# Optimization experiments

Hardware: AMD Instinct MI355X
Metric: run time of the kernel (lower is better)

The kernel has to match this reference:

```python
import jax, jax.numpy as jnp
import numpy as np

B, N, DIM, H, K = 2, 8192, 256, 8, 32
HD = DIM // H


def setup_inputs() -> dict:
    key = jax.random.key(0)
    ks = jax.random.split(key, 10)
    s = 1.0 / np.sqrt(DIM)
    return {
        "x": jax.random.normal(ks[0], (B, N, DIM), jnp.float32),
        "xyz": jax.random.normal(ks[1], (B, N, 3), jnp.float32),
        "idx": jax.random.randint(ks[2], (B, N, K), 0, N, jnp.int32),
        "Wq": jax.random.normal(ks[3], (DIM, DIM), jnp.float32) * s,
        "bq": jnp.zeros((DIM,), jnp.float32),
        "Wk": jax.random.normal(ks[4], (DIM, DIM), jnp.float32) * s,
        "bk": jnp.zeros((DIM,), jnp.float32),
        "Wv": jax.random.normal(ks[5], (DIM, DIM), jnp.float32) * s,
        "bv": jnp.zeros((DIM,), jnp.float32),
        "Wo": jax.random.normal(ks[6], (DIM, DIM), jnp.float32) * s,
        "bo": jnp.zeros((DIM,), jnp.float32),
        "W1": jax.random.normal(ks[7], (3, 32), jnp.float32) * 0.5,
        "b1": jnp.zeros((32,), jnp.float32),
        "W2": jax.random.normal(ks[8], (32, H), jnp.float32) * 0.2,
        "b2": jnp.zeros((H,), jnp.float32),
    }


def reference(x, xyz, idx, Wq, bq, Wk, bk, Wv, bv, Wo, bo, W1, b1, W2, b2):
    Bn, Nn, C = x.shape
    k = idx.shape[-1]
    q = (x @ Wq + bq).reshape(Bn, Nn, H, HD)          # [B,N,H,hd]
    kf = (x @ Wk + bk).reshape(Bn, Nn, H, HD)
    vf = (x @ Wv + bv).reshape(Bn, Nn, H, HD)
    # gather k neighbors per point (per-batch fancy indexing)
    gather = jax.vmap(lambda f, i: f[i])               # [N,H,hd],[N,k] -> [N,k,H,hd]
    kn = gather(kf, idx)                               # [B,N,k,H,hd]
    vn = gather(vf, idx)
    nxyz = jax.vmap(lambda p, i: p[i])(xyz, idx)       # [B,N,k,3]
    rel = xyz[:, :, None, :] - nxyz                    # [B,N,k,3]
    bias = jax.nn.relu(rel @ W1 + b1) @ W2 + b2        # [B,N,k,H]
    scores = jnp.einsum('bnhd,bnkhd->bnhk', q, kn) / np.sqrt(HD).astype(np.float32)
    scores = scores + bias.transpose(0, 1, 3, 2)       # [B,N,H,k]
    attn = jax.nn.softmax(scores, axis=-1)
    out = jnp.einsum('bnhk,bnkhd->bnhd', attn, vn).reshape(Bn, Nn, C)
    return out @ Wo + bo
```

## Files before the change

kernel.cpp:

```cpp
#include <hip/hip_runtime.h>
#include <hip/hip_bf16.h>

typedef unsigned int uint32;
typedef unsigned short ushort;
typedef __attribute__((ext_vector_type(4))) float floatx4;
typedef __attribute__((ext_vector_type(8))) __bf16 bf16x8;

#define NPTS 8192

__device__ __forceinline__ ushort f2bf(float f) {
    uint32 u = __float_as_uint(f);
    uint32 r = (u + 0x7fffu + ((u >> 16) & 1u)) >> 16;
    return (ushort)r;
}
__device__ __forceinline__ float bf1(ushort u) { return __uint_as_float((uint32)u << 16); }
__device__ __forceinline__ float bflo(uint32 u) { return __uint_as_float(u << 16); }
__device__ __forceinline__ float bfhi(uint32 u) { return __uint_as_float(u & 0xffff0000u); }

__global__ __launch_bounds__(256) void prep_kernel(
    const float* __restrict__ x, const float* __restrict__ xyz, const int* __restrict__ idx,
    const float* __restrict__ Wq, const float* __restrict__ Wk,
    const float* __restrict__ Wv, const float* __restrict__ Wo,
    const float* __restrict__ bq, const float* __restrict__ bk, const float* __restrict__ bv,
    const float* __restrict__ W1, const float* __restrict__ b1,
    const float* __restrict__ W2, const float* __restrict__ b2,
    ushort* __restrict__ xb, ushort* __restrict__ Wqkvt, ushort* __restrict__ Wot,
    float* __restrict__ biasqkv, ushort* __restrict__ bias_g) {
    const int bi = blockIdx.x;
    const int tid = threadIdx.x;
    if (bi < 4096) {
        int i = (bi * 256 + tid) * 4;
        float4 v = *(const float4*)(x + i);
        ushort4 o;
        o.x = f2bf(v.x); o.y = f2bf(v.y); o.z = f2bf(v.z); o.w = f2bf(v.w);
        *(ushort4*)(xb + i) = o;
    } else if (bi < 5120) {
        int f = (bi - 4096) * 256 + tid;
        if (f < 768 * 256) {
            int n = f >> 8, k = f & 255;
            int seg = n >> 8, nc = n & 255;
            const float* W = (seg == 0) ? Wq : (seg == 1) ? Wk : Wv;
            Wqkvt[f] = f2bf(W[k * 256 + nc]);
        } else {
            int g = f - 768 * 256;
            int n = g >> 8, k = g & 255;
            Wot[g] = f2bf(Wo[k * 256 + n]);
        }
        if (f < 768) biasqkv[f] = (f < 256) ? bq[f] : (f < 512) ? bk[f - 256] : bv[f - 512];
    } else {
        __shared__ float W1s[96], b1s[32], W2s[256], b2s[8];
        if (tid < 96) W1s[tid] = W1[tid];
        if (tid < 32) b1s[tid] = b1[tid];
        W2s[tid] = W2[tid];
        if (tid < 8) b2s[tid] = b2[tid];
        __syncthreads();
        const int wid = tid >> 6, lane = tid & 63;
        const int s = lane >> 5, j = lane & 31;
        const int p = (bi - 5120) * 8 + wid * 2 + s;
        const int b = p >> 13, n = p & 8191;
        const int nj = idx[(size_t)p * 32 + j];
        const size_t pb = ((size_t)b * NPTS + n) * 3;
        const size_t nb = ((size_t)b * NPTS + nj) * 3;
        const float rx = xyz[pb + 0] - xyz[nb + 0];
        const float ry = xyz[pb + 1] - xyz[nb + 1];
        const float rz = xyz[pb + 2] - xyz[nb + 2];
        float acc[8];
#pragma unroll
        for (int h = 0; h < 8; ++h) acc[h] = b2s[h];
#pragma unroll
        for (int u = 0; u < 32; ++u) {
            float hv = rx * W1s[u] + ry * W1s[32 + u] + rz * W1s[64 + u] + b1s[u];
            hv = fmaxf(hv, 0.f);
#pragma unroll
            for (int h = 0; h < 8; ++h) acc[h] += hv * W2s[u * 8 + h];
        }
#pragma unroll
        for (int h = 0; h < 8; ++h) bias_g[((size_t)p * 8 + h) * 32 + j] = f2bf(acc[h]);
    }
}

__global__ __launch_bounds__(256) void gemm_qkv(const ushort* __restrict__ A,
                                                const ushort* __restrict__ Wt,
                                                const float* __restrict__ bias,
                                                ushort* __restrict__ outp) {
    __shared__ __align__(16) ushort As[128 * 64];
    __shared__ __align__(16) ushort Bs[128 * 64];
    const int tid = threadIdx.x;
    const int w = tid >> 6, lane = tid & 63;
    const int m0 = blockIdx.y * 128, n0 = blockIdx.x * 128;
    const int wm = (w & 1) * 64, wn = (w >> 1) * 64;
    const int N = 768;

    floatx4 acc[4][4] = {};

    for (int kt = 0; kt < 256; kt += 64) {
        __syncthreads();
#pragma unroll
        for (int c4 = 0; c4 < 4; ++c4) {
            const int c = w * 4 + c4;
            const int r = c * 8 + (lane >> 3);
            const int gseg = (lane & 7) ^ (r & 7);
            const char* ga = (const char*)(A + (size_t)(m0 + r) * 256 + kt) + gseg * 16;
            const char* gb = (const char*)(Wt + (size_t)(n0 + r) * 256 + kt) + gseg * 16;
            __builtin_amdgcn_global_load_lds((const __attribute__((address_space(1))) void*)ga,
                                             (__attribute__((address_space(3))) void*)((char*)As + c * 1024),
                                             16, 0, 0);
            __builtin_amdgcn_global_load_lds((const __attribute__((address_space(1))) void*)gb,
                                             (__attribute__((address_space(3))) void*)((char*)Bs + c * 1024),
                                             16, 0, 0);
        }
        __syncthreads();

        bf16x8 af[2][4], bg[2][4];
#pragma unroll
        for (int kk = 0; kk < 2; ++kk) {
            const int s = kk * 4 + (lane >> 4);
            const int phys = s ^ (lane & 7);
#pragma unroll
            for (int i = 0; i < 4; ++i) {
                af[kk][i] = *(const bf16x8*)((const char*)As + (wm + i * 16 + (lane & 15)) * 128 + phys * 16);
                bg[kk][i] = *(const bf16x8*)((const char*)Bs + (wn + i * 16 + (lane & 15)) * 128 + phys * 16);
            }
        }
#pragma unroll
        for (int kk = 0; kk < 2; ++kk)
#pragma unroll
            for (int mi = 0; mi < 4; ++mi)
#pragma unroll
                for (int ni = 0; ni < 4; ++ni)
                    acc[mi][ni] = __builtin_amdgcn_mfma_f32_16x16x32_bf16(af[kk][mi], bg[kk][ni], acc[mi][ni], 0, 0, 0);
    }

#pragma unroll
    for (int ni = 0; ni < 4; ++ni) {
        const int col = n0 + wn + ni * 16 + (lane & 15);
        const float bv = bias[col];
#pragma unroll
        for (int mi = 0; mi < 4; ++mi) {
            const int row0 = m0 + wm + mi * 16 + (lane >> 4) * 4;
#pragma unroll
            for (int r = 0; r < 4; ++r)
                outp[(size_t)(row0 + r) * N + col] = f2bf(acc[mi][ni][r] + bv);
        }
    }
}

__global__ __launch_bounds__(256) void gemm_mfma64(const ushort* __restrict__ A,
                                                   const ushort* __restrict__ Wt,
                                                   const float* __restrict__ bias,
                                                   float* __restrict__ outv, int N) {
    __shared__ __align__(16) ushort As[64 * 32];
    __shared__ __align__(16) ushort Bs[64 * 32];
    const int tid = threadIdx.x;
    const int w = tid >> 6, lane = tid & 63;
    const int m0 = blockIdx.y * 64, n0 = blockIdx.x * 64;
    const int row = tid >> 2;
    const int col16 = (tid & 3) * 16;

    floatx4 acc[4] = {};

    for (int kt = 0; kt < 256; kt += 32) {
        __syncthreads();
        {
            const char* ga = (const char*)(A + (size_t)(m0 + row) * 256 + kt) + col16;
            const char* gb = (const char*)(Wt + (size_t)(n0 + row) * 256 + kt) + col16;
            __builtin_amdgcn_global_load_lds((const __attribute__((address_space(1))) void*)ga,
                                             (__attribute__((address_space(3))) void*)((char*)As + w * 1024),
                                             16, 0, 0);
            __builtin_amdgcn_global_load_lds((const __attribute__((address_space(1))) void*)gb,
                                             (__attribute__((address_space(3))) void*)((char*)Bs + w * 1024),
                                             16, 0, 0);
        }
        __syncthreads();

        bf16x8 af = *(const bf16x8*)&As[(w * 16 + (lane & 15)) * 32 + (lane >> 4) * 8];
        bf16x8 bg[4];
#pragma unroll
        for (int ni = 0; ni < 4; ++ni)
            bg[ni] = *(const bf16x8*)&Bs[(ni * 16 + (lane & 15)) * 32 + (lane >> 4) * 8];
#pragma unroll
        for (int ni = 0; ni < 4; ++ni)
            acc[ni] = __builtin_amdgcn_mfma_f32_16x16x32_bf16(af, bg[ni], acc[ni], 0, 0, 0);
    }

#pragma unroll
    for (int ni = 0; ni < 4; ++ni) {
        const int col = n0 + ni * 16 + (lane & 15);
        const float bv = bias[col];
        const int row0 = m0 + w * 16 + (lane >> 4) * 4;
#pragma unroll
        for (int r = 0; r < 4; ++r)
            outv[(size_t)(row0 + r) * N + col] = acc[ni][r] + bv;
    }
}

__global__ __launch_bounds__(256) void attn_kernel(
    const ushort* __restrict__ qkv, const int* __restrict__ idx,
    const ushort* __restrict__ bias_g, ushort* __restrict__ out) {
    __shared__ __align__(16) float q_s[4][2][32];
    __shared__ float e_s[4][2][32];
    __shared__ uint32 off_s[4][2][32];
    __shared__ float ssum_s[4][2];

    const int tid = threadIdx.x, wid = tid >> 6, lane = tid & 63;
    const int h = blockIdx.x & 7;
    const int pg = blockIdx.x >> 3;
    const int pbase = pg * 8 + wid * 2;
    const char* base = (const char*)qkv;

    const int s = lane >> 5, j = lane & 31;
    const int p = pbase + s;
    const int b = p >> 13;

    off_s[wid][s][j] = (uint32)(idx[(size_t)p * 32 + j] + b * NPTS) * 1536u;
    q_s[wid][s][j] = bf1(qkv[(size_t)p * 768 + h * 32 + j]);
    __syncthreads();

    {
        const uint4* kp = (const uint4*)(base + off_s[wid][s][j] + 512 + h * 64);
        float d = 0.f;
#pragma unroll
        for (int c = 0; c < 4; ++c) {
            uint4 kv = kp[c];
            float4 qa = *(const float4*)&q_s[wid][s][c * 8];
            float4 qb = *(const float4*)&q_s[wid][s][c * 8 + 4];
            d += bflo(kv.x) * qa.x + bfhi(kv.x) * qa.y
               + bflo(kv.y) * qa.z + bfhi(kv.y) * qa.w
               + bflo(kv.z) * qb.x + bfhi(kv.z) * qb.y
               + bflo(kv.w) * qb.z + bfhi(kv.w) * qb.w;
        }
        const float sc = d * 0.17677669529663687f + bf1(bias_g[((size_t)p * 8 + h) * 32 + j]);
        const float e = __expf(sc);
        float ssum = e;
#pragma unroll
        for (int msk = 16; msk >= 1; msk >>= 1) ssum += __shfl_xor(ssum, msk, 64);
        e_s[wid][s][j] = e;
        if (j == 0) ssum_s[wid][s] = ssum;
    }
    __syncthreads();

    {
        const int s2 = lane >> 5;
        const int q4 = (lane >> 3) & 3;
        const int j3 = lane & 7;
        const int p2 = pbase + s2;
        float a[8] = {};
#pragma unroll
        for (int t = 0; t < 4; ++t) {
            const int j2 = t * 8 + j3;
            const float wgt = e_s[wid][s2][j2];
            const uint4 v = *(const uint4*)(base + off_s[wid][s2][j2] + 1024 + h * 64 + q4 * 16);
            a[0] += wgt * bflo(v.x); a[1] += wgt * bfhi(v.x);
            a[2] += wgt * bflo(v.y); a[3] += wgt * bfhi(v.y);
            a[4] += wgt * bflo(v.z); a[5] += wgt * bfhi(v.z);
            a[6] += wgt * bflo(v.w); a[7] += wgt * bfhi(v.w);
        }
#pragma unroll
        for (int msk = 1; msk <= 4; msk <<= 1) {
#pragma unroll
            for (int d = 0; d < 8; ++d) a[d] += __shfl_xor(a[d], msk, 64);
        }
        if (j3 == 0) {
            const float rinv = __builtin_amdgcn_rcpf(ssum_s[wid][s2]);
            uint4 ov;
            ov.x = (uint32)f2bf(a[0] * rinv) | ((uint32)f2bf(a[1] * rinv) << 16);
            ov.y = (uint32)f2bf(a[2] * rinv) | ((uint32)f2bf(a[3] * rinv) << 16);
            ov.z = (uint32)f2bf(a[4] * rinv) | ((uint32)f2bf(a[5] * rinv) << 16);
            ov.w = (uint32)f2bf(a[6] * rinv) | ((uint32)f2bf(a[7] * rinv) << 16);
            *(uint4*)(out + (size_t)p2 * 256 + h * 32 + q4 * 8) = ov;
        }
    }
}

extern "C" void kernel_launch(void* const* d_in, const int* in_sizes, int n_in,
                              void* d_out, int out_size, void* d_ws, size_t ws_size,
                              hipStream_t stream) {
    const float* x   = (const float*)d_in[0];
    const float* xyz = (const float*)d_in[1];
    const int*   idx = (const int*)d_in[2];
    const float* Wq = (const float*)d_in[3];
    const float* bq = (const float*)d_in[4];
    const float* Wk = (const float*)d_in[5];
    const float* bk = (const float*)d_in[6];
    const float* Wv = (const float*)d_in[7];
    const float* bv = (const float*)d_in[8];
    const float* Wo = (const float*)d_in[9];
    const float* bo = (const float*)d_in[10];
    const float* W1 = (const float*)d_in[11];
    const float* b1 = (const float*)d_in[12];
    const float* W2 = (const float*)d_in[13];
    const float* b2 = (const float*)d_in[14];

    char* wsb = (char*)d_ws;
    ushort* x_bf    = (ushort*)wsb;
    ushort* aout_bf = x_bf;
    ushort* qkv_bf  = (ushort*)(wsb + 8388608);
    ushort* Wqkvt   = (ushort*)(wsb + 33554432);
    ushort* Wot     = (ushort*)(wsb + 33947648);
    float*  biasqkv = (float*)(wsb + 34078720);
    ushort* bias_g  = (ushort*)(wsb + 34081792);

    prep_kernel<<<7168, 256, 0, stream>>>(x, xyz, idx, Wq, Wk, Wv, Wo, bq, bk, bv,
                                          W1, b1, W2, b2, x_bf, Wqkvt, Wot, biasqkv, bias_g);

    gemm_qkv<<<dim3(6, 128), 256, 0, stream>>>(x_bf, Wqkvt, biasqkv, qkv_bf);

    attn_kernel<<<16384, 256, 0, stream>>>(qkv_bf, idx, bias_g, aout_bf);

    gemm_mfma64<<<dim3(4, 256), 256, 0, stream>>>(aout_bf, Wot, bo, (float*)d_out, 256);
}
```

Measured before the change: 198.4 us.

## Store Q/K/V and geometric bias head-major and schedule attention blocks by head

The QKV GEMM epilogue now writes Q, K and V into separate head-major buffers, and the prep kernel writes the geometric bias head-major too. Attention blocks are ordered so consecutive blocks share a head. The aim is for gathered K/V rows of one head (64 bytes each) to sit in a compact 1 MB region per head, which improves L2 locality for the random neighbour gathers. The V accumulation is also reworked to use 32-bit per-lane loads over 16 neighbours with a single shuffle instead of uint4 loads and a three-step shuffle reduction. The GEMM stores become more scattered, and the output writes become narrower.

```diff
diff --git a/kernel.cpp b/kernel.cpp
--- a/kernel.cpp
+++ b/kernel.cpp
@@ -7,6 +7,7 @@
 typedef __attribute__((ext_vector_type(8))) __bf16 bf16x8;
 
 #define NPTS 8192
+#define HSZ 524288
 
 __device__ __forceinline__ ushort f2bf(float f) {
     uint32 u = __float_as_uint(f);
@@ -25,7 +26,7 @@
     const float* __restrict__ W1, const float* __restrict__ b1,
     const float* __restrict__ W2, const float* __restrict__ b2,
     ushort* __restrict__ xb, ushort* __restrict__ Wqkvt, ushort* __restrict__ Wot,
-    float* __restrict__ biasqkv, ushort* __restrict__ bias_g) {
+    float* __restrict__ biasqkv, ushort* __restrict__ bias_hg) {
     const int bi = blockIdx.x;
     const int tid = threadIdx.x;
     if (bi < 4096) {
@@ -75,21 +76,21 @@
             for (int h = 0; h < 8; ++h) acc[h] += hv * W2s[u * 8 + h];
         }
 #pragma unroll
-        for (int h = 0; h < 8; ++h) bias_g[((size_t)p * 8 + h) * 32 + j] = f2bf(acc[h]);
+        for (int h = 0; h < 8; ++h) bias_hg[(size_t)h * HSZ + p * 32 + j] = f2bf(acc[h]);
     }
 }
 
 __global__ __launch_bounds__(256) void gemm_qkv(const ushort* __restrict__ A,
                                                 const ushort* __restrict__ Wt,
                                                 const float* __restrict__ bias,
-                                                ushort* __restrict__ outp) {
+                                                ushort* __restrict__ qh, ushort* __restrict__ kh,
+                                                ushort* __restrict__ vh) {
     __shared__ __align__(16) ushort As[128 * 64];
     __shared__ __align__(16) ushort Bs[128 * 64];
     const int tid = threadIdx.x;
     const int w = tid >> 6, lane = tid & 63;
     const int m0 = blockIdx.y * 128, n0 = blockIdx.x * 128;
     const int wm = (w & 1) * 64, wn = (w >> 1) * 64;
-    const int N = 768;
 
     floatx4 acc[4][4] = {};
 
@@ -134,13 +135,17 @@
 #pragma unroll
     for (int ni = 0; ni < 4; ++ni) {
         const int col = n0 + wn + ni * 16 + (lane & 15);
+        const int seg = col >> 8;
+        const int head = (col >> 5) & 7;
+        const int dim = col & 31;
+        ushort* segp = (seg == 0) ? qh : (seg == 1) ? kh : vh;
         const float bv = bias[col];
 #pragma unroll
         for (int mi = 0; mi < 4; ++mi) {
             const int row0 = m0 + wm + mi * 16 + (lane >> 4) * 4;
 #pragma unroll
             for (int r = 0; r < 4; ++r)
-                outp[(size_t)(row0 + r) * N + col] = f2bf(acc[mi][ni][r] + bv);
+                segp[(size_t)head * HSZ + (size_t)(row0 + r) * 32 + dim] = f2bf(acc[mi][ni][r] + bv);
         }
     }
 }
@@ -195,29 +200,31 @@
 }
 
 __global__ __launch_bounds__(256) void attn_kernel(
-    const ushort* __restrict__ qkv, const int* __restrict__ idx,
-    const ushort* __restrict__ bias_g, ushort* __restrict__ out) {
+    const ushort* __restrict__ qh, const ushort* __restrict__ kh, const ushort* __restrict__ vh,
+    const int* __restrict__ idx, const ushort* __restrict__ bias_hg, ushort* __restrict__ out) {
     __shared__ __align__(16) float q_s[4][2][32];
     __shared__ float e_s[4][2][32];
     __shared__ uint32 off_s[4][2][32];
     __shared__ float ssum_s[4][2];
 
     const int tid = threadIdx.x, wid = tid >> 6, lane = tid & 63;
-    const int h = blockIdx.x & 7;
-    const int pg = blockIdx.x >> 3;
+    const int h = blockIdx.x >> 11;
+    const int pg = blockIdx.x & 2047;
     const int pbase = pg * 8 + wid * 2;
-    const char* base = (const char*)qkv;
+
+    const char* kh_h = (const char*)(kh + (size_t)h * HSZ);
+    const char* vh_h = (const char*)(vh + (size_t)h * HSZ);
 
     const int s = lane >> 5, j = lane & 31;
     const int p = pbase + s;
     const int b = p >> 13;
 
-    off_s[wid][s][j] = (uint32)(idx[(size_t)p * 32 + j] + b * NPTS) * 1536u;
-    q_s[wid][s][j] = bf1(qkv[(size_t)p * 768 + h * 32 + j]);
+    off_s[wid][s][j] = (uint32)(idx[(size_t)p * 32 + j] + b * NPTS) * 64u;
+    q_s[wid][s][j] = bf1(qh[(size_t)h * HSZ + p * 32 + j]);
     __syncthreads();
 
     {
-        const uint4* kp = (const uint4*)(base + off_s[wid][s][j] + 512 + h * 64);
+        const uint4* kp = (const uint4*)(kh_h + off_s[wid][s][j]);
         float d = 0.f;
 #pragma unroll
         for (int c = 0; c < 4; ++c) {
@@ -229,7 +236,7 @@
                + bflo(kv.z) * qb.x + bfhi(kv.z) * qb.y
                + bflo(kv.w) * qb.z + bfhi(kv.w) * qb.w;
         }
-        const float sc = d * 0.17677669529663687f + bf1(bias_g[((size_t)p * 8 + h) * 32 + j]);
+        const float sc = d * 0.17677669529663687f + bf1(bias_hg[(size_t)h * HSZ + p * 32 + j]);
         const float e = __expf(sc);
         float ssum = e;
 #pragma unroll
@@ -240,34 +247,23 @@
     __syncthreads();
 
     {
-        const int s2 = lane >> 5;
-        const int q4 = (lane >> 3) & 3;
-        const int j3 = lane & 7;
+        const int s2 = lane >> 5, hj = (lane >> 4) & 1, d2 = lane & 15;
         const int p2 = pbase + s2;
-        float a[8] = {};
-#pragma unroll
-        for (int t = 0; t < 4; ++t) {
-            const int j2 = t * 8 + j3;
+        const float rinv = __builtin_amdgcn_rcpf(ssum_s[wid][s2]);
+        float ax = 0.f, ay = 0.f;
+#pragma unroll
+        for (int jj = 0; jj < 16; ++jj) {
+            const int j2 = hj * 16 + jj;
             const float wgt = e_s[wid][s2][j2];
-            const uint4 v = *(const uint4*)(base + off_s[wid][s2][j2] + 1024 + h * 64 + q4 * 16);
-            a[0] += wgt * bflo(v.x); a[1] += wgt * bfhi(v.x);
-            a[2] += wgt * bflo(v.y); a[3] += wgt * bfhi(v.y);
-            a[4] += wgt * bflo(v.z); a[5] += wgt * bfhi(v.z);
-            a[6] += wgt * bflo(v.w); a[7] += wgt * bfhi(v.w);
-        }
-#pragma unroll
-        for (int msk = 1; msk <= 4; msk <<= 1) {
-#pragma unroll
-            for (int d = 0; d < 8; ++d) a[d] += __shfl_xor(a[d], msk, 64);
-        }
-        if (j3 == 0) {
-            const float rinv = __builtin_amdgcn_rcpf(ssum_s[wid][s2]);
-            uint4 ov;
-            ov.x = (uint32)f2bf(a[0] * rinv) | ((uint32)f2bf(a[1] * rinv) << 16);
-            ov.y = (uint32)f2bf(a[2] * rinv) | ((uint32)f2bf(a[3] * rinv) << 16);
-            ov.z = (uint32)f2bf(a[4] * rinv) | ((uint32)f2bf(a[5] * rinv) << 16);
-            ov.w = (uint32)f2bf(a[6] * rinv) | ((uint32)f2bf(a[7] * rinv) << 16);
-            *(uint4*)(out + (size_t)p2 * 256 + h * 32 + q4 * 8) = ov;
+            const uint32 v = *(const uint32*)(vh_h + off_s[wid][s2][j2] + d2 * 4);
+            ax += wgt * bflo(v);
+            ay += wgt * bfhi(v);
+        }
+        ax += __shfl_xor(ax, 16, 64);
+        ay += __shfl_xor(ay, 16, 64);
+        if (hj == 0) {
+            const uint32 o = (uint32)f2bf(ax * rinv) | ((uint32)f2bf(ay * rinv) << 16);
+            *(uint32*)(out + (size_t)p2 * 256 + h * 32 + d2 * 2) = o;
         }
     }
 }
@@ -294,18 +290,20 @@
     char* wsb = (char*)d_ws;
     ushort* x_bf    = (ushort*)wsb;
     ushort* aout_bf = x_bf;
-    ushort* qkv_bf  = (ushort*)(wsb + 8388608);
-    ushort* Wqkvt   = (ushort*)(wsb + 33554432);
-    ushort* Wot     = (ushort*)(wsb + 33947648);
-    float*  biasqkv = (float*)(wsb + 34078720);
-    ushort* bias_g  = (ushort*)(wsb + 34081792);
+    ushort* qh      = (ushort*)(wsb + 8388608);
+    ushort* kh      = (ushort*)(wsb + 16777216);
+    ushort* vh      = (ushort*)(wsb + 25165824);
+    ushort* bias_hg = (ushort*)(wsb + 33554432);
+    ushort* Wqkvt   = (ushort*)(wsb + 41943040);
+    ushort* Wot     = (ushort*)(wsb + 42336256);
+    float*  biasqkv = (float*)(wsb + 42467328);
 
     prep_kernel<<<7168, 256, 0, stream>>>(x, xyz, idx, Wq, Wk, Wv, Wo, bq, bk, bv,
-                                          W1, b1, W2, b2, x_bf, Wqkvt, Wot, biasqkv, bias_g);
-
-    gemm_qkv<<<dim3(6, 128), 256, 0, stream>>>(x_bf, Wqkvt, biasqkv, qkv_bf);
-
-    attn_kernel<<<16384, 256, 0, stream>>>(qkv_bf, idx, bias_g, aout_bf);
+                                          W1, b1, W2, b2, x_bf, Wqkvt, Wot, biasqkv, bias_hg);
+
+    gemm_qkv<<<dim3(6, 128), 256, 0, stream>>>(x_bf, Wqkvt, biasqkv, qh, kh, vh);
+
+    attn_kernel<<<16384, 256, 0, stream>>>(qh, kh, vh, idx, bias_hg, aout_bf);
 
     gemm_mfma64<<<dim3(4, 256), 256, 0, stream>>>(aout_bf, Wot, bo, (float*)d_out, 256);
 }
```

Measured after the change: 184.4 us. 1.08x faster.
